# Kernel tuning notes

Measured on AMD Instinct MI355X. Metric: run time of the kernel, lower is better.

## Reference

```python
import jax, jax.numpy as jnp
import numpy as np
import math

B, S, D, H, TD = 256, 200, 64, 512, 8


def setup_inputs():
    key = jax.random.key(0)
    ks = jax.random.split(key, 12)
    sd, sh, so = 1.0 / math.sqrt(D), 1.0 / math.sqrt(H), 1.0 / math.sqrt(H + TD)
    return dict(
        x=jax.random.normal(ks[0], (B, S, D), jnp.float32),
        a=jax.random.normal(ks[3], (B, TD), jnp.float32),
        t=jnp.cumsum(jax.random.uniform(ks[2], (B, S), jnp.float32), axis=1),
        mask=(jax.random.uniform(ks[1], (B, S, D)) < 0.8).astype(jnp.float32),
        w_dg_x=jax.random.normal(ks[4], (D,), jnp.float32) * sd,
        b_dg_x=jnp.zeros((D,), jnp.float32),
        W_dg_h=jax.random.normal(ks[5], (H, D), jnp.float32) * sd,
        b_dg_h=jnp.zeros((H,), jnp.float32),
        W=jax.random.normal(ks[6], (3 * H, D), jnp.float32) * sd,
        U=jax.random.normal(ks[7], (3 * H, H), jnp.float32) * sh,
        V=jax.random.normal(ks[8], (3 * H, D), jnp.float32) * sd,
        b=jnp.zeros((3 * H,), jnp.float32),
        attn_v=jnp.ones((H,), jnp.float32),
        W_out=jax.random.normal(ks[9], (H, H + TD), jnp.float32) * so,
        b_out=jnp.zeros((H,), jnp.float32),
    )


def reference(x, a, t, mask, w_dg_x, b_dg_x, W_dg_h, b_dg_h, W, U, V, b, attn_v, W_out, b_out):
    # ---- GRU-D preprocessing: per-feature time gaps delta ----
    x_tm = jnp.transpose(x, (1, 0, 2))    # (S,B,D) time-major
    m_tm = jnp.transpose(mask, (1, 0, 2))
    dt = jnp.diff(t, axis=1, prepend=t[:, :1])      # (B,S), dt[0]=0
    dt_tm = jnp.transpose(dt)[:, :, None]           # (S,B,1)
    # delta[i] = dt[i] + (1 - mask[i-1]) * delta[i-1]; ones at step 0 -> delta[0]=0
    m_prev = jnp.concatenate([jnp.ones((1,) + m_tm.shape[1:], m_tm.dtype), m_tm[:-1]], axis=0)

    def delta_step(d, inp):
        dt_i, mp_i = inp
        d = dt_i + (1.0 - mp_i) * d
        return d, d

    _, delta_tm = jax.lax.scan(delta_step, jnp.zeros((B, D), x.dtype), (dt_tm, m_prev))

    # empirical mean of observed values for imputation
    x_mean = (mask * x).sum((0, 1)) / jnp.maximum(mask.sum((0, 1)), 1.0)  # (D,)

    Wz, Wr, Wh = W[:H], W[H:2 * H], W[2 * H:]
    Uz, Ur, Uh = U[:H], U[H:2 * H], U[2 * H:]
    Vz, Vr, Vh = V[:H], V[H:2 * H], V[2 * H:]
    bz, br, bh = b[:H], b[H:2 * H], b[2 * H:]

    def cell(carry, inp):
        h, x_last = carry
        x_i, m_i, d_i = inp                                        # (B,D) each
        gamma_x = jnp.exp(-jax.nn.relu(w_dg_x * d_i + b_dg_x))     # (B,D) input decay
        gamma_h = jnp.exp(-jax.nn.relu(d_i @ W_dg_h.T + b_dg_h))   # (B,H) hidden decay
        x_hat = m_i * x_i + (1.0 - m_i) * (gamma_x * x_last + (1.0 - gamma_x) * x_mean)
        h_dec = gamma_h * h
        z = jax.nn.sigmoid(x_hat @ Wz.T + h_dec @ Uz.T + m_i @ Vz.T + bz)
        r = jax.nn.sigmoid(x_hat @ Wr.T + h_dec @ Ur.T + m_i @ Vr.T + br)
        h_til = jnp.tanh(x_hat @ Wh.T + (r * h_dec) @ Uh.T + m_i @ Vh.T + bh)
        h_new = (1.0 - z) * h_dec + z * h_til
        x_last_new = m_i * x_i + (1.0 - m_i) * x_last
        return (h_new, x_last_new), h_new

    init = (jnp.zeros((B, H), x.dtype), jnp.zeros((B, D), x.dtype))
    _, h_all = jax.lax.scan(cell, init, (x_tm, m_tm, delta_tm))    # (S,B,H)

    # ---- attention pooling over time (softmax along seq dim, as in torch dim=0) ----
    score = (h_all @ attn_v) / math.sqrt(H)        # (S,B)
    w_attn = jax.nn.softmax(score, axis=0)
    attn_h = (h_all * w_attn[..., None]).sum(0)    # (B,H)

    # ---- treatment head ----
    return jnp.concatenate([attn_h, a], axis=1) @ W_out.T + b_out  # (B,H)
```

## Files before the change

kernel.cpp:

```cpp
#include <hip/hip_runtime.h>
#include <hip/hip_bf16.h>
#include <stdint.h>


typedef unsigned short u16;
typedef unsigned int   u32;
typedef unsigned long long u64;
typedef short bfrag  __attribute__((ext_vector_type(8)));
typedef u16   u16x8  __attribute__((ext_vector_type(8)));
typedef float f32x4  __attribute__((ext_vector_type(4)));

#define NB 256
#define NS 200
#define ND 64
#define NH 512

#define MFMA(a,b,c) __builtin_amdgcn_mfma_f32_16x16x32_bf16((a),(b),(c),0,0,0)

union UQ  { u16x8 h; bfrag s; u64 u[2]; uint4 q; };
union UF2 { float f[2]; u64 u; };

__device__ __forceinline__ float b2f(u16 v){ union { float f; u32 u; } c; c.u = ((u32)v) << 16; return c.f; }
__device__ __forceinline__ u16 f2b(float f){ union { float f; u32 u; } c; c.f = f; u32 r = c.u + 0x7FFFu + ((c.u >> 16) & 1u); return (u16)(r >> 16); }
__device__ __forceinline__ float sigm(float x){ return 1.f / (1.f + __expf(-x)); }
__device__ __forceinline__ float tanh_f(float x){ return 1.f - 2.f / (1.f + __expf(2.f * x)); }

__device__ __forceinline__ u64 cload64(const void* p){
  return __hip_atomic_load((const u64*)p, __ATOMIC_RELAXED, __HIP_MEMORY_SCOPE_AGENT);
}
__device__ __forceinline__ void cstore64(void* p, u64 v){
  __hip_atomic_store((u64*)p, v, __ATOMIC_RELAXED, __HIP_MEMORY_SCOPE_AGENT);
}
__device__ __forceinline__ bool spin_ge(u32* f, u32 tgt){
  int fuel = 1 << 19;
  while (__hip_atomic_load(f, __ATOMIC_RELAXED, __HIP_MEMORY_SCOPE_AGENT) < tgt) {
    __builtin_amdgcn_s_sleep(1);
    if (--fuel == 0) return false;
  }
  return true;
}
__device__ __forceinline__ void flag_add(u32* f){
  __hip_atomic_fetch_add(f, 1u, __ATOMIC_RELAXED, __HIP_MEMORY_SCOPE_AGENT);
}
__device__ __forceinline__ bfrag ldfrag(const float* src){
  f32x4 lo = *(const f32x4*)src;
  f32x4 hi = *(const f32x4*)(src + 4);
  UQ z;
  z.h[0]=f2b(lo[0]); z.h[1]=f2b(lo[1]); z.h[2]=f2b(lo[2]); z.h[3]=f2b(lo[3]);
  z.h[4]=f2b(hi[0]); z.h[5]=f2b(hi[1]); z.h[6]=f2b(hi[2]); z.h[7]=f2b(hi[3]);
  return z.s;
}


__global__ void transpose_k(const float* __restrict__ Wout, float* __restrict__ WT){
  int i = blockIdx.x * 256 + threadIdx.x;
  if (i < 520 * 512) { int k = i >> 9, ho = i & 511; WT[i] = Wout[ho * 520 + k]; }
}

__global__ void mean1_k(const float* __restrict__ x, const float* __restrict__ mask,
                        float* __restrict__ PX, float* __restrict__ PM){
  int s = blockIdx.x, tid = threadIdx.x;
  __shared__ float lx[256], lm[256];
  float xa = 0.f, ma = 0.f;
  for (int i = tid; i < NB * ND; i += 256) {
    int b = i >> 6, d = i & 63;
    size_t ix = ((size_t)b * NS + s) * 64 + d;
    float m = mask[ix];
    xa += m * x[ix]; ma += m;
  }
  lx[tid] = xa; lm[tid] = ma;
  __syncthreads();
  if (tid < 64) {
    PX[(size_t)s * 64 + tid] = lx[tid] + lx[tid + 64] + lx[tid + 128] + lx[tid + 192];
    PM[(size_t)s * 64 + tid] = lm[tid] + lm[tid + 64] + lm[tid + 128] + lm[tid + 192];
  }
}

__global__ void mean2_k(const float* __restrict__ PX, const float* __restrict__ PM,
                        float* __restrict__ XMEAN){
  int d = threadIdx.x;
  float sx = 0.f, sm = 0.f;
  for (int s = 0; s < NS; ++s){ sx += PX[s * 64 + d]; sm += PM[s * 64 + d]; }
  XMEAN[d] = sx / fmaxf(sm, 1.f);
}

__global__ void prep_k(const float* __restrict__ x, const float* __restrict__ mask,
                       const float* __restrict__ tc, const float* __restrict__ wdgx,
                       const float* __restrict__ bdgx, const float* __restrict__ XMEAN,
                       u16* __restrict__ XHAT, u16* __restrict__ MASKB, u16* __restrict__ DELTA){
  int g = blockIdx.x * 256 + threadIdx.x;
  int b = g >> 6, d = g & 63;
  float xmean = XMEAN[d], wx = wdgx[d], bx = bdgx[d];
  float xl = 0.f, del = 0.f, tprev = 0.f, mprev = 1.f;
  for (int s = 0; s < NS; ++s){
    float tv = tc[b * NS + s];
    float dtv = (s == 0) ? 0.f : (tv - tprev);
    tprev = tv;
    del = dtv + (1.f - mprev) * del;
    size_t ix = ((size_t)b * NS + s) * 64 + d;
    float m = mask[ix], xv = x[ix];
    float gx = __expf(-fmaxf(0.f, wx * del + bx));
    float xh = m * xv + (1.f - m) * (gx * xl + (1.f - gx) * xmean);
    size_t ox = ((size_t)s * NB + b) * 64 + d;
    XHAT[ox] = f2b(xh); MASKB[ox] = f2b(m); DELTA[ox] = f2b(del);
    xl = m * xv + (1.f - m) * xl;
    mprev = m;
  }
}

__global__ __launch_bounds__(256, 1) void grud_rnn(
    const float* __restrict__ Um, const float* __restrict__ Wm, const float* __restrict__ Vm,
    const float* __restrict__ bv, const float* __restrict__ Wdg, const float* __restrict__ bdg,
    const u16* __restrict__ XHAT, const u16* __restrict__ MASKB, const u16* __restrict__ DELTA,
    u16* __restrict__ HDECB, u16* __restrict__ RHB, u16* __restrict__ XPART,
    u16* __restrict__ GAMB, u16* __restrict__ HALL, u32* __restrict__ flags)
{
  const int tid = threadIdx.x, lane = tid & 63, wid = tid >> 6, bid = blockIdx.x;
  const int rb = bid / 7, role = bid % 7, m0 = rb * 16;
  const int l16 = lane & 15, krow = lane >> 4, r4 = lane >> 2, cb = (lane & 3) * 8;
  u32* FH = flags + rb * 128;
  u32* FR = flags + rb * 128 + 32;
  u32* FX = flags + rb * 128 + 64;
  u32* FG = flags + rb * 128 + 96;

  __shared__ u16 hpanel[64 * 16 * 8];
  __shared__ u16 rhpanel[64 * 16 * 8];
  __shared__ float xb[4][16 * 33];
  __shared__ int s_ab;
  float* xw = xb[wid];
  const f32x4 Z4 = {0.f, 0.f, 0.f, 0.f};
  if (tid == 0) s_ab = 0;
  __syncthreads();

  if (role < 4) {
    const int c0g = role * 128 + wid * 32;
    bfrag BUz[16][2], BUr[16][2], BUh[16][2];
    #pragma unroll
    for (int kk = 0; kk < 16; ++kk) {
      #pragma unroll
      for (int t2 = 0; t2 < 2; ++t2) {
        const size_t ko = (size_t)(kk * 32 + krow * 8);
        BUz[kk][t2] = ldfrag(Um + (size_t)(       c0g + t2 * 16 + l16) * 512 + ko);
        BUr[kk][t2] = ldfrag(Um + (size_t)(512  + c0g + t2 * 16 + l16) * 512 + ko);
        BUh[kk][t2] = ldfrag(Um + (size_t)(1024 + c0g + t2 * 16 + l16) * 512 + ko);
      }
    }

    for (int t = 0; t < NS; ++t) {
      const int slot = t & 1;
      if (tid == 0 && t > 0)  { if (!spin_ge(FH, 4u * (u32)t)) s_ab = 1; }
      if (tid == 64)          { if (!spin_ge(FX, 2u * (u32)(t + 1))) s_ab = 1; }
      if (tid == 128)         { u32 gt = (t + 1 < NS) ? (u32)(t + 1) : (u32)(NS - 1);
                                if (!spin_ge(FG, gt)) s_ab = 1; }
      __syncthreads();
      if (s_ab) break;
      const u16* xpb = XPART + (((size_t)slot * 16 + rb) * 16 + r4) * 1536;
      u64 xz0 = cload64(xpb + c0g + cb),        xz1 = cload64(xpb + c0g + cb + 4);
      u64 xr0 = cload64(xpb + 512 + c0g + cb),  xr1 = cload64(xpb + 512 + c0g + cb + 4);
      u64 xh0 = cload64(xpb + 1024 + c0g + cb), xh1 = cload64(xpb + 1024 + c0g + cb + 4);
      u64 gm0 = 0, gm1 = 0;
      if (t + 1 < NS) {
        const u16* gpb = GAMB + (((size_t)((t + 1) & 1) * 16 + rb) * 16 + r4) * 512 + c0g + cb;
        gm0 = cload64(gpb); gm1 = cload64(gpb + 4);
      }
      {
        const int srow = tid >> 4, sc = (tid & 15) * 32;
        u16* dp = &hpanel[((sc >> 3) * 16 + srow) * 8];
        if (t > 0) {
          const u16* hs = HDECB + (size_t)(m0 + srow) * 512 + sc;
          u64 a0 = cload64(hs),      a1 = cload64(hs + 4),  a2 = cload64(hs + 8),  a3 = cload64(hs + 12);
          u64 a4 = cload64(hs + 16), a5 = cload64(hs + 20), a6 = cload64(hs + 24), a7 = cload64(hs + 28);
          *(u64*)(dp)       = a0; *(u64*)(dp + 4)   = a1;
          *(u64*)(dp + 128) = a2; *(u64*)(dp + 132) = a3;
          *(u64*)(dp + 256) = a4; *(u64*)(dp + 260) = a5;
          *(u64*)(dp + 384) = a6; *(u64*)(dp + 388) = a7;
        } else {
          *(u64*)(dp)       = 0; *(u64*)(dp + 4)   = 0;
          *(u64*)(dp + 128) = 0; *(u64*)(dp + 132) = 0;
          *(u64*)(dp + 256) = 0; *(u64*)(dp + 260) = 0;
          *(u64*)(dp + 384) = 0; *(u64*)(dp + 388) = 0;
        }
      }
      __syncthreads();
      f32x4 ar0 = Z4, ar1 = Z4;
      #pragma unroll
      for (int kk = 0; kk < 16; ++kk) {
        bfrag a = *(const bfrag*)&hpanel[((kk * 4 + krow) * 16 + l16) * 8];
        ar0 = MFMA(a, BUr[kk][0], ar0); ar1 = MFMA(a, BUr[kk][1], ar1);
      }
      #pragma unroll
      for (int j = 0; j < 4; ++j) { xw[(krow*4+j)*33 + l16] = ar0[j]; xw[(krow*4+j)*33 + 16 + l16] = ar1[j]; }
      UQ xru; xru.u[0] = xr0; xru.u[1] = xr1;
      UQ hdu; hdu.h = *(const u16x8*)&hpanel[(((c0g + cb) >> 3) * 16 + r4) * 8];
      UQ rhv;
      #pragma unroll
      for (int q = 0; q < 8; ++q) {
        float rv = sigm(b2f(xru.h[q]) + xw[r4 * 33 + cb + q]);
        rhv.h[q] = f2b(rv * b2f(hdu.h[q]));
      }
      { u16* dst = RHB + (size_t)(m0 + r4) * 512 + c0g + cb;
        cstore64(dst, rhv.u[0]); cstore64(dst + 4, rhv.u[1]); }
      asm volatile("s_waitcnt vmcnt(0)" ::: "memory");
      __syncthreads();
      if (tid == 0) flag_add(FR);
      f32x4 az0 = Z4, az1 = Z4;
      #pragma unroll
      for (int kk = 0; kk < 16; ++kk) {
        bfrag a = *(const bfrag*)&hpanel[((kk * 4 + krow) * 16 + l16) * 8];
        az0 = MFMA(a, BUz[kk][0], az0); az1 = MFMA(a, BUz[kk][1], az1);
      }
      #pragma unroll
      for (int j = 0; j < 4; ++j) { xw[(krow*4+j)*33 + l16] = az0[j]; xw[(krow*4+j)*33 + 16 + l16] = az1[j]; }
      UQ xzu; xzu.u[0] = xz0; xzu.u[1] = xz1;
      float zz8[8];
      #pragma unroll
      for (int q = 0; q < 8; ++q) zz8[q] = sigm(b2f(xzu.h[q]) + xw[r4 * 33 + cb + q]);
      if (tid == 0) { if (!spin_ge(FR, 4u * (u32)(t + 1))) s_ab = 1; }
      __syncthreads();
      if (s_ab) break;
      {
        const int srow = tid >> 4, sc = (tid & 15) * 32;
        const u16* rs = RHB + (size_t)(m0 + srow) * 512 + sc;
        u64 a0 = cload64(rs),      a1 = cload64(rs + 4),  a2 = cload64(rs + 8),  a3 = cload64(rs + 12);
        u64 a4 = cload64(rs + 16), a5 = cload64(rs + 20), a6 = cload64(rs + 24), a7 = cload64(rs + 28);
        u16* dp = &rhpanel[((sc >> 3) * 16 + srow) * 8];
        *(u64*)(dp)       = a0; *(u64*)(dp + 4)   = a1;
        *(u64*)(dp + 128) = a2; *(u64*)(dp + 132) = a3;
        *(u64*)(dp + 256) = a4; *(u64*)(dp + 260) = a5;
        *(u64*)(dp + 384) = a6; *(u64*)(dp + 388) = a7;
      }
      __syncthreads();
      f32x4 ah0 = Z4, ah1 = Z4;
      #pragma unroll
      for (int kk = 0; kk < 16; ++kk) {
        bfrag a = *(const bfrag*)&rhpanel[((kk * 4 + krow) * 16 + l16) * 8];
        ah0 = MFMA(a, BUh[kk][0], ah0); ah1 = MFMA(a, BUh[kk][1], ah1);
      }
      #pragma unroll
      for (int j = 0; j < 4; ++j) { xw[(krow*4+j)*33 + l16] = ah0[j]; xw[(krow*4+j)*33 + 16 + l16] = ah1[j]; }
      UQ xhu; xhu.u[0] = xh0; xhu.u[1] = xh1;
      UQ hwv; float hn8[8];
      #pragma unroll
      for (int q = 0; q < 8; ++q) {
        float til = tanh_f(b2f(xhu.h[q]) + xw[r4 * 33 + cb + q]);
        float hdq = b2f(hdu.h[q]);
        float hv = (1.f - zz8[q]) * hdq + zz8[q] * til;
        hn8[q] = hv; hwv.h[q] = f2b(hv);
      }
      if (t + 1 < NS) {
        UQ gmu; gmu.u[0] = gm0; gmu.u[1] = gm1;
        UQ hdn;
        #pragma unroll
        for (int q = 0; q < 8; ++q) hdn.h[q] = f2b(b2f(gmu.h[q]) * hn8[q]);
        u16* dp2 = HDECB + (size_t)(m0 + r4) * 512 + c0g + cb;
        cstore64(dp2, hdn.u[0]); cstore64(dp2 + 4, hdn.u[1]);
      }
      asm volatile("s_waitcnt vmcnt(0)" ::: "memory");
      __syncthreads();
      if (tid == 0) flag_add(FH);
      *(uint4*)(HALL + ((size_t)t * NB + m0 + r4) * 512 + c0g + cb) = hwv.q;
    }
  } else if (role < 6) {
    const int p = role - 4;
    const int wbase = p * 768 + wid * 192;
    bfrag BW[12][2], BV2[12][2];
    #pragma unroll
    for (int ct = 0; ct < 12; ++ct)
      #pragma unroll
      for (int kx = 0; kx < 2; ++kx) {
        BW[ct][kx]  = ldfrag(Wm + (size_t)(wbase + ct * 16 + l16) * 64 + kx * 32 + krow * 8);
        BV2[ct][kx] = ldfrag(Vm + (size_t)(wbase + ct * 16 + l16) * 64 + kx * 32 + krow * 8);
      }
    float bias6[6][8];
    #pragma unroll
    for (int grp = 0; grp < 6; ++grp)
      #pragma unroll
      for (int q = 0; q < 8; ++q) bias6[grp][q] = bv[wbase + grp * 32 + cb + q];

    for (int t = 0; t < NS; ++t) {
      if (tid == 0 && t >= 2) { if (!spin_ge(FH, 4u * (u32)(t - 1))) s_ab = 1; }
      { const int kb = tid >> 4, row = tid & 15;
        const u16* sp = (kb < 8 ? XHAT : MASKB) + ((size_t)t * NB + m0 + row) * 64 + (kb & 7) * 8;
        *(uint4*)&hpanel[(kb * 16 + row) * 8] = *(const uint4*)sp; }
      __syncthreads();
      if (s_ab) break;
      u16* orow_ = XPART + (((size_t)(t & 1) * 16 + rb) * 16 + r4) * 1536 + wbase;
      #pragma unroll
      for (int grp = 0; grp < 6; ++grp) {
        f32x4 ac0 = Z4, ac1 = Z4;
        #pragma unroll
        for (int kx = 0; kx < 2; ++kx) {
          bfrag ax = *(const bfrag*)&hpanel[((kx * 4 + krow) * 16 + l16) * 8];
          ac0 = MFMA(ax, BW[grp*2][kx], ac0); ac1 = MFMA(ax, BW[grp*2+1][kx], ac1);
          bfrag am = *(const bfrag*)&hpanel[((8 + kx * 4 + krow) * 16 + l16) * 8];
          ac0 = MFMA(am, BV2[grp*2][kx], ac0); ac1 = MFMA(am, BV2[grp*2+1][kx], ac1);
        }
        #pragma unroll
        for (int j = 0; j < 4; ++j) { xw[(krow*4+j)*33 + l16] = ac0[j]; xw[(krow*4+j)*33 + 16 + l16] = ac1[j]; }
        UQ ov;
        #pragma unroll
        for (int q = 0; q < 8; ++q) ov.h[q] = f2b(xw[r4 * 33 + cb + q] + bias6[grp][q]);
        cstore64(orow_ + grp * 32 + cb, ov.u[0]); cstore64(orow_ + grp * 32 + cb + 4, ov.u[1]);
      }
      asm volatile("s_waitcnt vmcnt(0)" ::: "memory");
      __syncthreads();
      if (tid == 0) flag_add(FX);
    }
  } else {
    bfrag BG[8][2];
    #pragma unroll
    for (int ct = 0; ct < 8; ++ct)
      #pragma unroll
      for (int kx = 0; kx < 2; ++kx)
        BG[ct][kx] = ldfrag(Wdg + (size_t)(wid * 128 + ct * 16 + l16) * 64 + kx * 32 + krow * 8);
    float gb4[4][8];
    #pragma unroll
    for (int grp = 0; grp < 4; ++grp)
      #pragma unroll
      for (int q = 0; q < 8; ++q) gb4[grp][q] = bdg[wid * 128 + grp * 32 + cb + q];

    for (int tt = 1; tt < NS; ++tt) {
      if (tid == 0 && tt >= 3) { if (!spin_ge(FH, 4u * (u32)(tt - 2))) s_ab = 1; }
      if (tid < 128) {
        const int kb = tid >> 4, row = tid & 15;
        const u16* sp = DELTA + ((size_t)tt * NB + m0 + row) * 64 + kb * 8;
        *(uint4*)&hpanel[(kb * 16 + row) * 8] = *(const uint4*)sp;
      }
      __syncthreads();
      if (s_ab) break;
      u16* orow_ = GAMB + (((size_t)(tt & 1) * 16 + rb) * 16 + r4) * 512 + wid * 128;
      #pragma unroll
      for (int grp = 0; grp < 4; ++grp) {
        f32x4 ac0 = Z4, ac1 = Z4;
        #pragma unroll
        for (int kx = 0; kx < 2; ++kx) {
          bfrag a = *(const bfrag*)&hpanel[((kx * 4 + krow) * 16 + l16) * 8];
          ac0 = MFMA(a, BG[grp*2][kx], ac0); ac1 = MFMA(a, BG[grp*2+1][kx], ac1);
        }
        #pragma unroll
        for (int j = 0; j < 4; ++j) { xw[(krow*4+j)*33 + l16] = ac0[j]; xw[(krow*4+j)*33 + 16 + l16] = ac1[j]; }
        UQ ov;
        #pragma unroll
        for (int q = 0; q < 8; ++q)
          ov.h[q] = f2b(__expf(-fmaxf(0.f, xw[r4 * 33 + cb + q] + gb4[grp][q])));
        cstore64(orow_ + grp * 32 + cb, ov.u[0]); cstore64(orow_ + grp * 32 + cb + 4, ov.u[1]);
      }
      asm volatile("s_waitcnt vmcnt(0)" ::: "memory");
      __syncthreads();
      if (tid == 0) flag_add(FG);
    }
  }
}


__global__ void attn_k(const u16* __restrict__ HALL, const float* __restrict__ av,
                       float* __restrict__ ATTN){
  const int b = blockIdx.x, tid = threadIdx.x, lane = tid & 63, wid = tid >> 6;
  __shared__ float avs[512], wgt[256], red[8];
  for (int i = tid; i < 512; i += 256) avs[i] = av[i];
  __syncthreads();
  float val = -3.0e38f;
  if (tid < NS) {
    const u16* hp = HALL + ((size_t)tid * NB + b) * 512;
    float acc = 0.f;
    for (int h = 0; h < 512; h += 8) {
      UQ w; w.q = *(const uint4*)(hp + h);
      #pragma unroll
      for (int j = 0; j < 8; ++j) acc += b2f(w.h[j]) * avs[h + j];
    }
    val = acc * 0.04419417382415922f;
  }
  float m = val;
  #pragma unroll
  for (int off = 32; off; off >>= 1) m = fmaxf(m, __shfl_xor(m, off, 64));
  if (lane == 0) red[wid] = m;
  __syncthreads();
  m = fmaxf(fmaxf(red[0], red[1]), fmaxf(red[2], red[3]));
  float e = (tid < NS) ? __expf(val - m) : 0.f;
  float sum = e;
  #pragma unroll
  for (int off = 32; off; off >>= 1) sum += __shfl_xor(sum, off, 64);
  if (lane == 0) red[4 + wid] = sum;
  __syncthreads();
  const float ssum = red[4] + red[5] + red[6] + red[7];
  wgt[tid] = e / ssum;
  __syncthreads();
  float a0 = 0.f, a1 = 0.f;
  const int h0 = tid * 2;
  for (int s = 0; s < NS; ++s) {
    float w = wgt[s];
    u32 pr = *(const u32*)(HALL + ((size_t)s * NB + b) * 512 + h0);
    a0 += w * b2f((u16)(pr & 0xFFFFu));
    a1 += w * b2f((u16)(pr >> 16));
  }
  ATTN[(size_t)b * 512 + h0] = a0;
  ATTN[(size_t)b * 512 + h0 + 1] = a1;
}

__global__ void out_k(const float* __restrict__ ATTN, const float* __restrict__ Ain,
                      const float* __restrict__ WT, const float* __restrict__ bout,
                      float* __restrict__ OUT){
  const int g = blockIdx.x, tid = threadIdx.x;
  __shared__ float ah[4][520];
  for (int i = tid; i < 4 * 520; i += 256) {
    int bb = i / 520, k = i % 520;
    int b = g * 4 + bb;
    ah[bb][k] = (k < 512) ? ATTN[(size_t)b * 512 + k] : Ain[b * 8 + (k - 512)];
  }
  __syncthreads();
  #pragma unroll
  for (int part = 0; part < 2; ++part) {
    const int ho = part * 256 + tid;
    float a0 = bout[ho], a1 = a0, a2 = a0, a3 = a0;
    for (int k = 0; k < 520; ++k) {
      float w = WT[(size_t)k * 512 + ho];
      a0 += ah[0][k] * w; a1 += ah[1][k] * w; a2 += ah[2][k] * w; a3 += ah[3][k] * w;
    }
    OUT[(size_t)(g * 4 + 0) * 512 + ho] = a0;
    OUT[(size_t)(g * 4 + 1) * 512 + ho] = a1;
    OUT[(size_t)(g * 4 + 2) * 512 + ho] = a2;
    OUT[(size_t)(g * 4 + 3) * 512 + ho] = a3;
  }
}


extern "C" void kernel_launch(void* const* d_in, const int* in_sizes, int n_in,
                              void* d_out, int out_size, void* d_ws, size_t ws_size,
                              hipStream_t stream) {
  (void)in_sizes; (void)n_in; (void)out_size; (void)ws_size;
  const float* x    = (const float*)d_in[0];
  const float* a_in = (const float*)d_in[1];
  const float* tc   = (const float*)d_in[2];
  const float* mask = (const float*)d_in[3];
  const float* wdgx = (const float*)d_in[4];
  const float* bdgx = (const float*)d_in[5];
  const float* Wdgh = (const float*)d_in[6];
  const float* bdgh = (const float*)d_in[7];
  const float* Wm   = (const float*)d_in[8];
  const float* Um   = (const float*)d_in[9];
  const float* Vm   = (const float*)d_in[10];
  const float* bvv  = (const float*)d_in[11];
  const float* attv = (const float*)d_in[12];
  const float* Wout = (const float*)d_in[13];
  const float* bout = (const float*)d_in[14];

  char* ws = (char*)d_ws;
  size_t o = 0;
  auto al = [&](size_t sz) { size_t r = o; o += (sz + 255) & ~(size_t)255; return r; };
  u32*   flags = (u32*)  (ws + al(16 * 128 * 4));
  float* XMEAN = (float*)(ws + al(256));
  float* PX    = (float*)(ws + al((size_t)NS * 64 * 4));
  float* PM    = (float*)(ws + al((size_t)NS * 64 * 4));
  u16*   XHAT  = (u16*)  (ws + al((size_t)NS * NB * 64 * 2));
  u16*   MASKB = (u16*)  (ws + al((size_t)NS * NB * 64 * 2));
  u16*   DELTA = (u16*)  (ws + al((size_t)NS * NB * 64 * 2));
  u16*   HDECB = (u16*)  (ws + al((size_t)NB * NH * 2));
  u16*   RHB   = (u16*)  (ws + al((size_t)NB * NH * 2));
  u16*   XPART = (u16*)  (ws + al((size_t)2 * 16 * 16 * 1536 * 2));
  u16*   GAMB  = (u16*)  (ws + al((size_t)2 * 16 * 16 * 512 * 2));
  u16*   HALL  = (u16*)  (ws + al((size_t)NS * NB * NH * 2));
  float* ATTN  = (float*)(ws + al((size_t)NB * NH * 4));
  float* WT    = (float*)(ws + al((size_t)520 * 512 * 4));

  hipMemsetAsync(flags, 0, 16 * 128 * 4, stream);

  transpose_k<<<(520 * 512 + 255) / 256, 256, 0, stream>>>(Wout, WT);
  mean1_k<<<NS, 256, 0, stream>>>(x, mask, PX, PM);
  mean2_k<<<1, 64, 0, stream>>>(PX, PM, XMEAN);
  prep_k<<<NB * ND / 256, 256, 0, stream>>>(x, mask, tc, wdgx, bdgx, XMEAN, XHAT, MASKB, DELTA);
  grud_rnn<<<112, 256, 0, stream>>>(Um, Wm, Vm, bvv, Wdgh, bdgh, XHAT, MASKB, DELTA,
                                    HDECB, RHB, XPART, GAMB, HALL, flags);
  attn_k<<<NB, 256, 0, stream>>>(HALL, attv, ATTN);
  out_k<<<64, 256, 0, stream>>>(ATTN, a_in, WT, bout, (float*)d_out);
}
```

Before: 1.934 ms.

## Spread recurrent GRU-D work over more blocks with per-wave flags and direct fragment loads

The recurrent U-matmul work per batch-row group moves from 4 blocks to 8 (grid grows from 112 to 176 blocks), so each wave now owns 16 hidden columns instead of 32. Block-wide __syncthreads and atomic counters are replaced by per-wave monotonic flag stores, and each wave polls all producer flags at once with a wave-wide vote. MFMA A-fragments for h_dec and r*h are loaded straight from global memory into registers instead of being staged in shared memory. The aim is to shorten the per-timestep critical path and spread the serial recurrence over more CUs, in exchange for more flag traffic and redundant global loads of the hidden-state panel.

```diff
diff --git a/kernel.cpp b/kernel.cpp
--- a/kernel.cpp
+++ b/kernel.cpp
@@ -31,16 +31,21 @@
 __device__ __forceinline__ void cstore64(void* p, u64 v){
   __hip_atomic_store((u64*)p, v, __ATOMIC_RELAXED, __HIP_MEMORY_SCOPE_AGENT);
 }
-__device__ __forceinline__ bool spin_ge(u32* f, u32 tgt){
-  int fuel = 1 << 19;
-  while (__hip_atomic_load(f, __ATOMIC_RELAXED, __HIP_MEMORY_SCOPE_AGENT) < tgt) {
-    __builtin_amdgcn_s_sleep(1);
+__device__ __forceinline__ u32 cload32(const u32* p){
+  return __hip_atomic_load(p, __ATOMIC_RELAXED, __HIP_MEMORY_SCOPE_AGENT);
+}
+__device__ __forceinline__ void cstore32(u32* p, u32 v){
+  __hip_atomic_store(p, v, __ATOMIC_RELAXED, __HIP_MEMORY_SCOPE_AGENT);
+}
+__device__ __forceinline__ bool spin_vec(const u32* base, int widx, u32 tgt){
+  const u32* p = base + widx;
+  int fuel = 1 << 21;
+  while (true) {
+    u32 v = cload32(p);
+    if (__all(v >= tgt)) return true;
+    __builtin_amdgcn_s_sleep(2);
     if (--fuel == 0) return false;
   }
-  return true;
-}
-__device__ __forceinline__ void flag_add(u32* f){
-  __hip_atomic_fetch_add(f, 1u, __ATOMIC_RELAXED, __HIP_MEMORY_SCOPE_AGENT);
 }
 __device__ __forceinline__ bfrag ldfrag(const float* src){
   f32x4 lo = *(const f32x4*)src;
@@ -116,15 +121,15 @@
     u16* __restrict__ GAMB, u16* __restrict__ HALL, u32* __restrict__ flags)
 {
   const int tid = threadIdx.x, lane = tid & 63, wid = tid >> 6, bid = blockIdx.x;
-  const int rb = bid / 7, role = bid % 7, m0 = rb * 16;
-  const int l16 = lane & 15, krow = lane >> 4, r4 = lane >> 2, cb = (lane & 3) * 8;
+  const int rb = bid / 11, role = bid % 11, m0 = rb * 16;
+  const int l16 = lane & 15, krow = lane >> 4;
+  const int r4 = lane >> 2, c4 = (lane & 3) * 4, cb = (lane & 3) * 8;
   u32* FH = flags + rb * 128;
-  u32* FR = flags + rb * 128 + 32;
-  u32* FX = flags + rb * 128 + 64;
-  u32* FG = flags + rb * 128 + 96;
-
-  __shared__ u16 hpanel[64 * 16 * 8];
-  __shared__ u16 rhpanel[64 * 16 * 8];
+  u32* FR = FH + 32;
+  u32* FX = FH + 64;
+  u32* FG = FH + 80;
+
+  __shared__ u16 hpanel[16 * 16 * 8];
   __shared__ float xb[4][16 * 33];
   __shared__ int s_ab;
   float* xw = xb[wid];
@@ -132,136 +137,98 @@
   if (tid == 0) s_ab = 0;
   __syncthreads();
 
-  if (role < 4) {
-    const int c0g = role * 128 + wid * 32;
-    bfrag BUz[16][2], BUr[16][2], BUh[16][2];
+  if (role < 8) {
+    const int gw = role * 4 + wid;
+    const int cw = role * 64 + wid * 16;
+    bfrag BUz[16], BUr[16], BUh[16];
     #pragma unroll
     for (int kk = 0; kk < 16; ++kk) {
-      #pragma unroll
-      for (int t2 = 0; t2 < 2; ++t2) {
-        const size_t ko = (size_t)(kk * 32 + krow * 8);
-        BUz[kk][t2] = ldfrag(Um + (size_t)(       c0g + t2 * 16 + l16) * 512 + ko);
-        BUr[kk][t2] = ldfrag(Um + (size_t)(512  + c0g + t2 * 16 + l16) * 512 + ko);
-        BUh[kk][t2] = ldfrag(Um + (size_t)(1024 + c0g + t2 * 16 + l16) * 512 + ko);
-      }
+      const size_t ko = (size_t)(kk * 32 + krow * 8);
+      BUz[kk] = ldfrag(Um + (size_t)(       cw + l16) * 512 + ko);
+      BUr[kk] = ldfrag(Um + (size_t)(512  + cw + l16) * 512 + ko);
+      BUh[kk] = ldfrag(Um + (size_t)(1024 + cw + l16) * 512 + ko);
     }
 
     for (int t = 0; t < NS; ++t) {
-      const int slot = t & 1;
-      if (tid == 0 && t > 0)  { if (!spin_ge(FH, 4u * (u32)t)) s_ab = 1; }
-      if (tid == 64)          { if (!spin_ge(FX, 2u * (u32)(t + 1))) s_ab = 1; }
-      if (tid == 128)         { u32 gt = (t + 1 < NS) ? (u32)(t + 1) : (u32)(NS - 1);
-                                if (!spin_ge(FG, gt)) s_ab = 1; }
-      __syncthreads();
-      if (s_ab) break;
-      const u16* xpb = XPART + (((size_t)slot * 16 + rb) * 16 + r4) * 1536;
-      u64 xz0 = cload64(xpb + c0g + cb),        xz1 = cload64(xpb + c0g + cb + 4);
-      u64 xr0 = cload64(xpb + 512 + c0g + cb),  xr1 = cload64(xpb + 512 + c0g + cb + 4);
-      u64 xh0 = cload64(xpb + 1024 + c0g + cb), xh1 = cload64(xpb + 1024 + c0g + cb + 4);
-      u64 gm0 = 0, gm1 = 0;
+      if (!spin_vec(FX, lane & 1, (u32)(t + 1))) return;
+      const u16* xpb = XPART + (((size_t)(t & 1) * 16 + rb) * 16 + r4) * 1536 + cw + c4;
+      u64 xzu = cload64(xpb);
+      u64 xru = cload64(xpb + 512);
+      u64 xhu = cload64(xpb + 1024);
+      u64 gmu = 0;
       if (t + 1 < NS) {
-        const u16* gpb = GAMB + (((size_t)((t + 1) & 1) * 16 + rb) * 16 + r4) * 512 + c0g + cb;
-        gm0 = cload64(gpb); gm1 = cload64(gpb + 4);
-      }
-      {
-        const int srow = tid >> 4, sc = (tid & 15) * 32;
-        u16* dp = &hpanel[((sc >> 3) * 16 + srow) * 8];
-        if (t > 0) {
-          const u16* hs = HDECB + (size_t)(m0 + srow) * 512 + sc;
-          u64 a0 = cload64(hs),      a1 = cload64(hs + 4),  a2 = cload64(hs + 8),  a3 = cload64(hs + 12);
-          u64 a4 = cload64(hs + 16), a5 = cload64(hs + 20), a6 = cload64(hs + 24), a7 = cload64(hs + 28);
-          *(u64*)(dp)       = a0; *(u64*)(dp + 4)   = a1;
-          *(u64*)(dp + 128) = a2; *(u64*)(dp + 132) = a3;
-          *(u64*)(dp + 256) = a4; *(u64*)(dp + 260) = a5;
-          *(u64*)(dp + 384) = a6; *(u64*)(dp + 388) = a7;
-        } else {
-          *(u64*)(dp)       = 0; *(u64*)(dp + 4)   = 0;
-          *(u64*)(dp + 128) = 0; *(u64*)(dp + 132) = 0;
-          *(u64*)(dp + 256) = 0; *(u64*)(dp + 260) = 0;
-          *(u64*)(dp + 384) = 0; *(u64*)(dp + 388) = 0;
+        if (!spin_vec(FG, 0, (u32)(t + 1))) return;
+        gmu = cload64(GAMB + (((size_t)((t + 1) & 1) * 16 + rb) * 16 + r4) * 512 + cw + c4);
+      }
+      UQ HA[16]; u64 hdu = 0;
+      if (t > 0) {
+        if (!spin_vec(FH, lane & 31, (u32)t)) return;
+        hdu = cload64(HDECB + (size_t)(m0 + r4) * 512 + cw + c4);
+        #pragma unroll
+        for (int kk = 0; kk < 16; ++kk) {
+          const u16* p = HDECB + (size_t)(m0 + l16) * 512 + kk * 32 + krow * 8;
+          HA[kk].u[0] = cload64(p); HA[kk].u[1] = cload64(p + 4);
         }
-      }
-      __syncthreads();
-      f32x4 ar0 = Z4, ar1 = Z4;
+      } else {
+        #pragma unroll
+        for (int kk = 0; kk < 16; ++kk) { HA[kk].u[0] = 0; HA[kk].u[1] = 0; }
+      }
+      f32x4 ar = Z4;
+      #pragma unroll
+      for (int kk = 0; kk < 16; ++kk) ar = MFMA(HA[kk].s, BUr[kk], ar);
+      #pragma unroll
+      for (int j = 0; j < 4; ++j) xw[(krow * 4 + j) * 17 + l16] = ar[j];
+      UQ xr_; xr_.u[0] = xru; UQ hd_; hd_.u[0] = hdu;
+      UQ rh_;
+      #pragma unroll
+      for (int q = 0; q < 4; ++q) {
+        float rv = sigm(b2f(xr_.h[q]) + xw[r4 * 17 + c4 + q]);
+        rh_.h[q] = f2b(rv * b2f(hd_.h[q]));
+      }
+      cstore64(RHB + (size_t)(m0 + r4) * 512 + cw + c4, rh_.u[0]);
+      asm volatile("s_waitcnt vmcnt(0)" ::: "memory");
+      if (lane == 0) cstore32(FR + gw, (u32)(t + 1));
+      f32x4 az = Z4;
+      #pragma unroll
+      for (int kk = 0; kk < 16; ++kk) az = MFMA(HA[kk].s, BUz[kk], az);
+      #pragma unroll
+      for (int j = 0; j < 4; ++j) xw[(krow * 4 + j) * 17 + l16] = az[j];
+      UQ xz_; xz_.u[0] = xzu;
+      float zz[4];
+      #pragma unroll
+      for (int q = 0; q < 4; ++q) zz[q] = sigm(b2f(xz_.h[q]) + xw[r4 * 17 + c4 + q]);
+      if (!spin_vec(FR, lane & 31, (u32)(t + 1))) return;
+      UQ RA[16];
       #pragma unroll
       for (int kk = 0; kk < 16; ++kk) {
-        bfrag a = *(const bfrag*)&hpanel[((kk * 4 + krow) * 16 + l16) * 8];
-        ar0 = MFMA(a, BUr[kk][0], ar0); ar1 = MFMA(a, BUr[kk][1], ar1);
-      }
-      #pragma unroll
-      for (int j = 0; j < 4; ++j) { xw[(krow*4+j)*33 + l16] = ar0[j]; xw[(krow*4+j)*33 + 16 + l16] = ar1[j]; }
-      UQ xru; xru.u[0] = xr0; xru.u[1] = xr1;
-      UQ hdu; hdu.h = *(const u16x8*)&hpanel[(((c0g + cb) >> 3) * 16 + r4) * 8];
-      UQ rhv;
-      #pragma unroll
-      for (int q = 0; q < 8; ++q) {
-        float rv = sigm(b2f(xru.h[q]) + xw[r4 * 33 + cb + q]);
-        rhv.h[q] = f2b(rv * b2f(hdu.h[q]));
-      }
-      { u16* dst = RHB + (size_t)(m0 + r4) * 512 + c0g + cb;
-        cstore64(dst, rhv.u[0]); cstore64(dst + 4, rhv.u[1]); }
+        const u16* p = RHB + (size_t)(m0 + l16) * 512 + kk * 32 + krow * 8;
+        RA[kk].u[0] = cload64(p); RA[kk].u[1] = cload64(p + 4);
+      }
+      f32x4 ah = Z4;
+      #pragma unroll
+      for (int kk = 0; kk < 16; ++kk) ah = MFMA(RA[kk].s, BUh[kk], ah);
+      #pragma unroll
+      for (int j = 0; j < 4; ++j) xw[(krow * 4 + j) * 17 + l16] = ah[j];
+      UQ xh_; xh_.u[0] = xhu; UQ gm_; gm_.u[0] = gmu;
+      UQ hw_, hdn_;
+      float hn[4];
+      #pragma unroll
+      for (int q = 0; q < 4; ++q) {
+        float til = tanh_f(b2f(xh_.h[q]) + xw[r4 * 17 + c4 + q]);
+        hn[q] = (1.f - zz[q]) * b2f(hd_.h[q]) + zz[q] * til;
+        hw_.h[q] = f2b(hn[q]);
+      }
+      if (t + 1 < NS) {
+        #pragma unroll
+        for (int q = 0; q < 4; ++q) hdn_.h[q] = f2b(b2f(gm_.h[q]) * hn[q]);
+        cstore64(HDECB + (size_t)(m0 + r4) * 512 + cw + c4, hdn_.u[0]);
+      }
       asm volatile("s_waitcnt vmcnt(0)" ::: "memory");
-      __syncthreads();
-      if (tid == 0) flag_add(FR);
-      f32x4 az0 = Z4, az1 = Z4;
-      #pragma unroll
-      for (int kk = 0; kk < 16; ++kk) {
-        bfrag a = *(const bfrag*)&hpanel[((kk * 4 + krow) * 16 + l16) * 8];
-        az0 = MFMA(a, BUz[kk][0], az0); az1 = MFMA(a, BUz[kk][1], az1);
-      }
-      #pragma unroll
-      for (int j = 0; j < 4; ++j) { xw[(krow*4+j)*33 + l16] = az0[j]; xw[(krow*4+j)*33 + 16 + l16] = az1[j]; }
-      UQ xzu; xzu.u[0] = xz0; xzu.u[1] = xz1;
-      float zz8[8];
-      #pragma unroll
-      for (int q = 0; q < 8; ++q) zz8[q] = sigm(b2f(xzu.h[q]) + xw[r4 * 33 + cb + q]);
-      if (tid == 0) { if (!spin_ge(FR, 4u * (u32)(t + 1))) s_ab = 1; }
-      __syncthreads();
-      if (s_ab) break;
-      {
-        const int srow = tid >> 4, sc = (tid & 15) * 32;
-        const u16* rs = RHB + (size_t)(m0 + srow) * 512 + sc;
-        u64 a0 = cload64(rs),      a1 = cload64(rs + 4),  a2 = cload64(rs + 8),  a3 = cload64(rs + 12);
-        u64 a4 = cload64(rs + 16), a5 = cload64(rs + 20), a6 = cload64(rs + 24), a7 = cload64(rs + 28);
-        u16* dp = &rhpanel[((sc >> 3) * 16 + srow) * 8];
-        *(u64*)(dp)       = a0; *(u64*)(dp + 4)   = a1;
-        *(u64*)(dp + 128) = a2; *(u64*)(dp + 132) = a3;
-        *(u64*)(dp + 256) = a4; *(u64*)(dp + 260) = a5;
-        *(u64*)(dp + 384) = a6; *(u64*)(dp + 388) = a7;
-      }
-      __syncthreads();
-      f32x4 ah0 = Z4, ah1 = Z4;
-      #pragma unroll
-      for (int kk = 0; kk < 16; ++kk) {
-        bfrag a = *(const bfrag*)&rhpanel[((kk * 4 + krow) * 16 + l16) * 8];
-        ah0 = MFMA(a, BUh[kk][0], ah0); ah1 = MFMA(a, BUh[kk][1], ah1);
-      }
-      #pragma unroll
-      for (int j = 0; j < 4; ++j) { xw[(krow*4+j)*33 + l16] = ah0[j]; xw[(krow*4+j)*33 + 16 + l16] = ah1[j]; }
-      UQ xhu; xhu.u[0] = xh0; xhu.u[1] = xh1;
-      UQ hwv; float hn8[8];
-      #pragma unroll
-      for (int q = 0; q < 8; ++q) {
-        float til = tanh_f(b2f(xhu.h[q]) + xw[r4 * 33 + cb + q]);
-        float hdq = b2f(hdu.h[q]);
-        float hv = (1.f - zz8[q]) * hdq + zz8[q] * til;
-        hn8[q] = hv; hwv.h[q] = f2b(hv);
-      }
-      if (t + 1 < NS) {
-        UQ gmu; gmu.u[0] = gm0; gmu.u[1] = gm1;
-        UQ hdn;
-        #pragma unroll
-        for (int q = 0; q < 8; ++q) hdn.h[q] = f2b(b2f(gmu.h[q]) * hn8[q]);
-        u16* dp2 = HDECB + (size_t)(m0 + r4) * 512 + c0g + cb;
-        cstore64(dp2, hdn.u[0]); cstore64(dp2 + 4, hdn.u[1]);
-      }
-      asm volatile("s_waitcnt vmcnt(0)" ::: "memory");
-      __syncthreads();
-      if (tid == 0) flag_add(FH);
-      *(uint4*)(HALL + ((size_t)t * NB + m0 + r4) * 512 + c0g + cb) = hwv.q;
-    }
-  } else if (role < 6) {
-    const int p = role - 4;
+      if (lane == 0) cstore32(FH + gw, (u32)(t + 1));
+      *(u64*)(HALL + ((size_t)t * NB + m0 + r4) * 512 + cw + c4) = hw_.u[0];
+    }
+  } else if (role < 10) {
+    const int p = role - 8;
     const int wbase = p * 768 + wid * 192;
     bfrag BW[12][2], BV2[12][2];
     #pragma unroll
@@ -278,7 +245,8 @@
       for (int q = 0; q < 8; ++q) bias6[grp][q] = bv[wbase + grp * 32 + cb + q];
 
     for (int t = 0; t < NS; ++t) {
-      if (tid == 0 && t >= 2) { if (!spin_ge(FH, 4u * (u32)(t - 1))) s_ab = 1; }
+      bool ok = (t < 2) || spin_vec(FH, lane & 31, (u32)(t - 1));
+      if (!ok) s_ab = 1;
       { const int kb = tid >> 4, row = tid & 15;
         const u16* sp = (kb < 8 ? XHAT : MASKB) + ((size_t)t * NB + m0 + row) * 64 + (kb & 7) * 8;
         *(uint4*)&hpanel[(kb * 16 + row) * 8] = *(const uint4*)sp; }
@@ -304,7 +272,7 @@
       }
       asm volatile("s_waitcnt vmcnt(0)" ::: "memory");
       __syncthreads();
-      if (tid == 0) flag_add(FX);
+      if (tid == 0) cstore32(FX + p, (u32)(t + 1));
     }
   } else {
     bfrag BG[8][2];
@@ -320,7 +288,8 @@
       for (int q = 0; q < 8; ++q) gb4[grp][q] = bdg[wid * 128 + grp * 32 + cb + q];
 
     for (int tt = 1; tt < NS; ++tt) {
-      if (tid == 0 && tt >= 3) { if (!spin_ge(FH, 4u * (u32)(tt - 2))) s_ab = 1; }
+      bool ok = (tt < 3) || spin_vec(FH, lane & 31, (u32)(tt - 2));
+      if (!ok) s_ab = 1;
       if (tid < 128) {
         const int kb = tid >> 4, row = tid & 15;
         const u16* sp = DELTA + ((size_t)tt * NB + m0 + row) * 64 + kb * 8;
@@ -347,7 +316,7 @@
       }
       asm volatile("s_waitcnt vmcnt(0)" ::: "memory");
       __syncthreads();
-      if (tid == 0) flag_add(FG);
+      if (tid == 0) cstore32(FG, (u32)tt);
     }
   }
 }
@@ -468,7 +437,7 @@
   mean1_k<<<NS, 256, 0, stream>>>(x, mask, PX, PM);
   mean2_k<<<1, 64, 0, stream>>>(PX, PM, XMEAN);
   prep_k<<<NB * ND / 256, 256, 0, stream>>>(x, mask, tc, wdgx, bdgx, XMEAN, XHAT, MASKB, DELTA);
-  grud_rnn<<<112, 256, 0, stream>>>(Um, Wm, Vm, bvv, Wdgh, bdgh, XHAT, MASKB, DELTA,
+  grud_rnn<<<176, 256, 0, stream>>>(Um, Wm, Vm, bvv, Wdgh, bdgh, XHAT, MASKB, DELTA,
                                     HDECB, RHB, XPART, GAMB, HALL, flags);
   attn_k<<<NB, 256, 0, stream>>>(HALL, attv, ATTN);
   out_k<<<64, 256, 0, stream>>>(ATTN, a_in, WT, bout, (float*)d_out);
```

After: 2.632 ms. +36.1%, slower.
